# Kernel optimization log

Hardware: AMD Instinct MI355X
Metric: run time of the kernel (lower is better)

Reference implementation:

```python
import jax, jax.numpy as jnp
import numpy as np

EPS = 1e-6
N, D = 8192, 256


def setup_inputs() -> dict:
    key = jax.random.key(0)
    kq, kc = jax.random.split(key)
    # scale 0.05 keeps points inside the Poincare ball: c*||q||^2 ~ 0.06 << 1
    query = jax.random.normal(kq, (N, D), dtype=jnp.float32) * 0.05
    c = jnp.asarray(0.1, dtype=jnp.float32)  # learnable curvature param (init 0.1)
    return {"query": query, "c": c}


def reference(query, c):
    # Self-attention path of HyperbolicAttention (keys = values = query).
    clamp_c = jnp.maximum(c, EPS)
    # ||u-v||^2 = ||u||^2 + ||v||^2 - 2 u.v  (same math as explicit expand+subtract,
    # but via a single GEMM instead of an (N, N, D) intermediate)
    qn = jnp.sum(query * query, axis=-1)                       # (N,)
    gram = query @ query.T                                     # (N, N)
    diff_sq = jnp.maximum(qn[:, None] + qn[None, :] - 2.0 * gram, 0.0)
    t = jnp.maximum(1.0 - clamp_c * qn, EPS)                   # clamped 1 - c||x||^2
    denom = t[:, None] * t[None, :]                            # (N, N)
    arg = jnp.maximum(1.0 + 2.0 * clamp_c * diff_sq / denom, 1.0 + EPS) + EPS
    dist = jnp.arccosh(arg) / jnp.sqrt(clamp_c)                # (N, N)
    attn = jax.nn.softmax(-dist, axis=-1)                      # (N, N)
    return attn @ query                                        # (N, D)
```

## Files before the change

### kernel.cpp

```cpp
#include <hip/hip_runtime.h>
#include <math.h>

#define NN 8192
#define DD 256
#define EPSV 1e-6f
#define BM 128
#define BN 64
#define CSPLIT 4
#define COLS_PER_BLOCK (NN / CSPLIT)
#define NJT (COLS_PER_BLOCK / BN)
#define PSTR 72
#define TSTR 266
#define SMEM_BYTES (32768 * 3 + BM * PSTR * 2)

typedef __bf16 bf16x8 __attribute__((ext_vector_type(8)));
typedef float f32x16 __attribute__((ext_vector_type(16)));
typedef unsigned short ushort;
typedef unsigned int uint;


__device__ inline ushort f2bf(float x) {
    uint u = __float_as_uint(x);
    u += 0x7fffu + ((u >> 16) & 1u);
    return (ushort)(u >> 16);
}

__device__ inline void gload_lds16(const void* g, void* l) {
    __builtin_amdgcn_global_load_lds((const __attribute__((address_space(1))) uint*)g,
                                     (__attribute__((address_space(3))) uint*)l, 16, 0, 0);
}

__global__ void zero_kernel(float* __restrict__ p) {
    int i = blockIdx.x * 256 + threadIdx.x;
    ((float4*)p)[i] = make_float4(0.f, 0.f, 0.f, 0.f);
}

__global__ void prep_kernel(const float* __restrict__ q, const float* __restrict__ cp,
                            ushort* __restrict__ qbf, ushort* __restrict__ qbfT,
                            float* __restrict__ qn, float* __restrict__ itv2) {
    __shared__ ushort T[64 * TSTR];
    const int t = threadIdx.x;
    const int p0 = blockIdx.x * 64;
    const int pr = t >> 2, fq = t & 3;
    const int row = p0 + pr;
    const float4* src = (const float4*)(q + (size_t)row * DD + fq * 64);
    ushort loc[64];
    float ss = 0.f;
    #pragma unroll
    for (int i = 0; i < 16; ++i) {
        float4 v = src[i];
        ushort b0 = f2bf(v.x), b1 = f2bf(v.y), b2 = f2bf(v.z), b3 = f2bf(v.w);
        loc[i * 4 + 0] = b0; loc[i * 4 + 1] = b1; loc[i * 4 + 2] = b2; loc[i * 4 + 3] = b3;
        float r0 = __uint_as_float((uint)b0 << 16), r1 = __uint_as_float((uint)b1 << 16);
        float r2 = __uint_as_float((uint)b2 << 16), r3 = __uint_as_float((uint)b3 << 16);
        ss += r0 * r0 + r1 * r1 + r2 * r2 + r3 * r3;
    }
    #pragma unroll
    for (int k = 0; k < 8; ++k)
        *(uint4*)(qbf + (size_t)row * DD + (((fq * 8 + k) ^ (row & 7)) * 8)) = *(uint4*)&loc[k * 8];
    #pragma unroll
    for (int k = 0; k < 32; ++k)
        *(ushort2*)&T[pr * TSTR + fq * 64 + k * 2] = *(ushort2*)&loc[k * 2];
    ss += __shfl_xor(ss, 1, 64);
    ss += __shfl_xor(ss, 2, 64);
    if (fq == 0) {
        float cc = fmaxf(cp[0], EPSV);
        qn[row] = ss;
        float tt = fmaxf(1.0f - cc * ss, EPSV);
        itv2[row] = sqrtf(2.0f * cc) / tt;
    }
    __syncthreads();
    #pragma unroll
    for (int pass = 0; pass < 4; ++pass) {
        int f = pass * 64 + (t >> 2);
        int quarter = t & 3;
        ushort tmp[16];
        #pragma unroll
        for (int i = 0; i < 16; ++i) tmp[i] = T[(quarter * 16 + i) * TSTR + f];
        *(uint4*)(qbfT + (size_t)f * NN + p0 + quarter * 16) = *(uint4*)&tmp[0];
        *(uint4*)(qbfT + (size_t)f * NN + p0 + quarter * 16 + 8) = *(uint4*)&tmp[8];
    }
}

__global__ __launch_bounds__(512, 2) void flash_kernel(
    const ushort* __restrict__ qbf, const ushort* __restrict__ qbfT,
    const float* __restrict__ cp, const float* __restrict__ qn,
    const float* __restrict__ itv2, float* __restrict__ Oacc, float* __restrict__ lacc) {
    extern __shared__ char smem[];
    ushort* Ktlds = (ushort*)(smem + 65536);
    ushort* Plds = (ushort*)(smem + 98304);

    const int tid = threadIdx.x;
    const int lane = tid & 63;
    const int w = tid >> 6;
    const int l31 = lane & 31;
    const int lhi = lane >> 5;
    const int qr = w >> 1;
    const int qc = w & 1;
    const int R0 = blockIdx.y * BM;
    const int C0 = blockIdx.x * COLS_PER_BLOCK;

    const float cc = fmaxf(cp[0], EPSV);
    const float rsc = rsqrtf(cc);

    const int rowA = R0 + qr * 32 + l31;
    const ushort* qrow = qbf + (size_t)rowA * DD;
    bf16x8 qa[16];
    #pragma unroll
    for (int kk = 0; kk < 16; ++kk) {
        int c = kk * 2 + lhi;
        qa[kk] = *(const bf16x8*)(qrow + ((c ^ (rowA & 7)) * 8));
    }

    float qnr16[16], itr16[16];
    #pragma unroll
    for (int r = 0; r < 16; ++r) {
        int row = R0 + qr * 32 + (r & 3) + 8 * (r >> 2) + 4 * lhi;
        qnr16[r] = qn[row];
        itr16[r] = itv2[row];
    }

    f32x16 o[4];
    #pragma unroll
    for (int ct = 0; ct < 4; ++ct)
        #pragma unroll
        for (int i = 0; i < 16; ++i) o[ct][i] = 0.f;
    float racc[16];
    #pragma unroll
    for (int r = 0; r < 16; ++r) racc[r] = 0.f;

    {
        const char* g = (const char*)(qbf + (size_t)C0 * DD);
        #pragma unroll
        for (int i = 0; i < 4; ++i) {
            int base = i * 8192 + w * 1024;
            gload_lds16(g + base + lane * 16, smem + base);
        }
    }

    #pragma unroll 1
    for (int jt = 0; jt < NJT; ++jt) {
        const int C = C0 + jt * BN;
        const ushort* Kc = (const ushort*)(smem + (jt & 1) * 32768);
        __syncthreads();

        if (jt + 1 < NJT) {
            const char* g = (const char*)(qbf + (size_t)(C + BN) * DD);
            char* dst = smem + ((jt + 1) & 1) * 32768;
            #pragma unroll
            for (int i = 0; i < 4; ++i) {
                int base = i * 8192 + w * 1024;
                gload_lds16(g + base + lane * 16, dst + base);
            }
        }
        {
            #pragma unroll
            for (int i = 0; i < 4; ++i) {
                int f0 = i * 64 + w * 8;
                int f = f0 + (lane >> 3);
                const char* g = (const char*)(qbfT + (size_t)f * NN + C) +
                                (((lane & 7) ^ (f & 7)) * 16);
                gload_lds16(g, (char*)Ktlds + f0 * 128);
            }
        }

        f32x16 s;
        #pragma unroll
        for (int i = 0; i < 16; ++i) s[i] = 0.f;
        const int jrow = qc * 32 + l31;
        const ushort* krow = Kc + jrow * DD;
        #pragma unroll
        for (int kk = 0; kk < 16; ++kk) {
            int c = kk * 2 + lhi;
            bf16x8 b = *(const bf16x8*)(krow + ((c ^ (jrow & 7)) * 8));
            s = __builtin_amdgcn_mfma_f32_32x32x16_bf16(qa[kk], b, s, 0, 0, 0);
        }

        {
            int J = C + jrow;
            float qnj = qn[J];
            float itj = itv2[J];
            #pragma unroll
            for (int r = 0; r < 16; ++r) {
                int mloc = qr * 32 + (r & 3) + 8 * (r >> 2) + 4 * lhi;
                float diff = fmaxf(qnr16[r] + qnj - 2.0f * s[r], 0.0f);
                float u = diff * itr16[r] * itj;
                float z = fmaxf(1.0f + u, 1.0f + EPSV) + EPSV;
                float y = z + sqrtf(fmaf(z, z, -1.0f));
                float p = __builtin_amdgcn_exp2f(-rsc * __builtin_amdgcn_logf(y));
                racc[r] += p;
                Plds[mloc * PSTR + jrow] = f2bf(p);
            }
        }
        __syncthreads();

        #pragma unroll
        for (int kt = 0; kt < 4; ++kt) {
            bf16x8 pa = *(const bf16x8*)&Plds[(qr * 32 + l31) * PSTR + kt * 16 + 8 * lhi];
            #pragma unroll
            for (int ct = 0; ct < 4; ++ct) {
                int f = qc * 128 + ct * 32 + l31;
                int cj = kt * 2 + lhi;
                bf16x8 vb = *(const bf16x8*)(Ktlds + f * 64 + (((cj ^ (f & 7))) * 8));
                o[ct] = __builtin_amdgcn_mfma_f32_32x32x16_bf16(pa, vb, o[ct], 0, 0, 0);
            }
        }
    }

    #pragma unroll
    for (int ct = 0; ct < 4; ++ct) {
        #pragma unroll
        for (int r = 0; r < 16; ++r) {
            int row = R0 + qr * 32 + (r & 3) + 8 * (r >> 2) + 4 * lhi;
            int d = qc * 128 + ct * 32 + l31;
            atomicAdd(&Oacc[(size_t)row * DD + d], o[ct][r]);
        }
    }
    #pragma unroll
    for (int off = 1; off <= 16; off <<= 1)
        #pragma unroll
        for (int r = 0; r < 16; ++r) racc[r] += __shfl_xor(racc[r], off, 64);
    if (l31 == 0) {
        #pragma unroll
        for (int r = 0; r < 16; ++r) {
            int row = R0 + qr * 32 + (r & 3) + 8 * (r >> 2) + 4 * lhi;
            atomicAdd(&lacc[row], racc[r]);
        }
    }
}

__global__ void norm_kernel(const float* __restrict__ Oacc, const float* __restrict__ lacc,
                            float* __restrict__ out) {
    int i = blockIdx.x * 256 + threadIdx.x;
    float4 v = ((const float4*)Oacc)[i];
    float inv = 1.0f / lacc[i >> 6];
    ((float4*)out)[i] = make_float4(v.x * inv, v.y * inv, v.z * inv, v.w * inv);
}

extern "C" void kernel_launch(void* const* d_in, const int* in_sizes, int n_in,
                              void* d_out, int out_size, void* d_ws, size_t ws_size,
                              hipStream_t stream) {
    (void)in_sizes; (void)n_in; (void)out_size; (void)ws_size;
    const float* q = (const float*)d_in[0];
    const float* cp = (const float*)d_in[1];
    float* out = (float*)d_out;
    float* ws = (float*)d_ws;
    float* Oacc = ws;
    float* lacc = ws + (size_t)NN * DD;
    float* qn = lacc + NN;
    float* itv2 = qn + NN;
    ushort* qbf = (ushort*)(itv2 + NN);
    ushort* qbfT = qbf + (size_t)NN * DD;

    (void)hipFuncSetAttribute((const void*)flash_kernel,
                              hipFuncAttributeMaxDynamicSharedMemorySize, SMEM_BYTES);

    zero_kernel<<<(NN * DD + NN) / 4 / 256, 256, 0, stream>>>(ws);
    prep_kernel<<<NN / 64, 256, 0, stream>>>(q, cp, qbf, qbfT, qn, itv2);
    flash_kernel<<<dim3(CSPLIT, NN / BM), 512, SMEM_BYTES, stream>>>(qbf, qbfT, cp, qn, itv2, Oacc, lacc);
    norm_kernel<<<(NN * DD / 4) / 256, 256, 0, stream>>>(Oacc, lacc, out);
}
```

Measured before the change: 205.6 us.

## Double-buffer transposed V tiles, retile PV GEMM, fuse zeroing into prep

The transposed-value tile is now double-buffered and prefetched one iteration ahead along with the key tile, so its global-to-LDS load no longer sits on the critical path before the PV MFMAs. The PV product is retiled so each wave computes a 2x2 block of 32x32 outputs, which reuses P and V fragments across MFMAs. The P buffer uses an XOR-swizzled layout instead of padding. The separate zero kernel is folded into the prep kernel to save a launch. The grid becomes 1D and the distance math is restructured with FMAs. LDS use rises to 144KB, which likely drops occupancy from 2 blocks to 1 per CU.

```diff
diff --git a/kernel.cpp b/kernel.cpp
--- a/kernel.cpp
+++ b/kernel.cpp
@@ -9,9 +9,8 @@
 #define CSPLIT 4
 #define COLS_PER_BLOCK (NN / CSPLIT)
 #define NJT (COLS_PER_BLOCK / BN)
-#define PSTR 72
 #define TSTR 266
-#define SMEM_BYTES (32768 * 3 + BM * PSTR * 2)
+#define SMEM_BYTES (65536 + 65536 + 16384)
 
 typedef __bf16 bf16x8 __attribute__((ext_vector_type(8)));
 typedef float f32x16 __attribute__((ext_vector_type(16)));
@@ -30,17 +29,19 @@
                                      (__attribute__((address_space(3))) uint*)l, 16, 0, 0);
 }
 
-__global__ void zero_kernel(float* __restrict__ p) {
-    int i = blockIdx.x * 256 + threadIdx.x;
-    ((float4*)p)[i] = make_float4(0.f, 0.f, 0.f, 0.f);
-}
-
 __global__ void prep_kernel(const float* __restrict__ q, const float* __restrict__ cp,
                             ushort* __restrict__ qbf, ushort* __restrict__ qbfT,
-                            float* __restrict__ qn, float* __restrict__ itv2) {
+                            float* __restrict__ qn, float* __restrict__ itv2,
+                            float* __restrict__ Oacc, float* __restrict__ lacc) {
     __shared__ ushort T[64 * TSTR];
     const int t = threadIdx.x;
-    const int p0 = blockIdx.x * 64;
+    const int b = blockIdx.x;
+    float4 z4 = make_float4(0.f, 0.f, 0.f, 0.f);
+    #pragma unroll
+    for (int i = 0; i < 16; ++i) ((float4*)Oacc)[b * 4096 + i * 256 + t] = z4;
+    if (t < 16) ((float4*)lacc)[b * 16 + t] = z4;
+
+    const int p0 = b * 64;
     const int pr = t >> 2, fq = t & 3;
     const int row = p0 + pr;
     const float4* src = (const float4*)(q + (size_t)row * DD + fq * 64);
@@ -87,8 +88,7 @@
     const float* __restrict__ cp, const float* __restrict__ qn,
     const float* __restrict__ itv2, float* __restrict__ Oacc, float* __restrict__ lacc) {
     extern __shared__ char smem[];
-    ushort* Ktlds = (ushort*)(smem + 65536);
-    ushort* Plds = (ushort*)(smem + 98304);
+    ushort* Plds = (ushort*)(smem + 131072);
 
     const int tid = threadIdx.x;
     const int lane = tid & 63;
@@ -97,11 +97,17 @@
     const int lhi = lane >> 5;
     const int qr = w >> 1;
     const int qc = w & 1;
-    const int R0 = blockIdx.y * BM;
-    const int C0 = blockIdx.x * COLS_PER_BLOCK;
+    const int qr2 = w >> 2;
+    const int fc = w & 3;
+
+    const int lid = blockIdx.x;
+    const int cs = lid & 3;
+    const int rb = lid >> 2;
+    const int R0 = rb * BM;
+    const int C0 = cs * COLS_PER_BLOCK;
 
     const float cc = fmaxf(cp[0], EPSV);
-    const float rsc = rsqrtf(cc);
+    const float nrsc = -rsqrtf(cc);
 
     const int rowA = R0 + qr * 32 + l31;
     const ushort* qrow = qbf + (size_t)rowA * DD;
@@ -120,11 +126,13 @@
         itr16[r] = itv2[row];
     }
 
-    f32x16 o[4];
-    #pragma unroll
-    for (int ct = 0; ct < 4; ++ct)
-        #pragma unroll
-        for (int i = 0; i < 16; ++i) o[ct][i] = 0.f;
+    f32x16 o[2][2];
+    #pragma unroll
+    for (int a = 0; a < 2; ++a)
+        #pragma unroll
+        for (int bb = 0; bb < 2; ++bb)
+            #pragma unroll
+            for (int i = 0; i < 16; ++i) o[a][bb][i] = 0.f;
     float racc[16];
     #pragma unroll
     for (int r = 0; r < 16; ++r) racc[r] = 0.f;
@@ -136,38 +144,49 @@
             int base = i * 8192 + w * 1024;
             gload_lds16(g + base + lane * 16, smem + base);
         }
+        #pragma unroll
+        for (int i = 0; i < 4; ++i) {
+            int f0 = i * 64 + w * 8;
+            int f = f0 + (lane >> 3);
+            const char* gk = (const char*)(qbfT + (size_t)f * NN + C0) +
+                             (((lane & 7) ^ (f & 7)) * 16);
+            gload_lds16(gk, smem + 65536 + f0 * 128);
+        }
     }
 
     #pragma unroll 1
     for (int jt = 0; jt < NJT; ++jt) {
         const int C = C0 + jt * BN;
-        const ushort* Kc = (const ushort*)(smem + (jt & 1) * 32768);
+        const int cur = jt & 1;
+        const ushort* Kc = (const ushort*)(smem + cur * 32768);
+        const ushort* Ktc = (const ushort*)(smem + 65536 + cur * 32768);
         __syncthreads();
 
         if (jt + 1 < NJT) {
+            const int nxt = cur ^ 1;
             const char* g = (const char*)(qbf + (size_t)(C + BN) * DD);
-            char* dst = smem + ((jt + 1) & 1) * 32768;
             #pragma unroll
             for (int i = 0; i < 4; ++i) {
                 int base = i * 8192 + w * 1024;
-                gload_lds16(g + base + lane * 16, dst + base);
-            }
-        }
-        {
+                gload_lds16(g + base + lane * 16, smem + nxt * 32768 + base);
+            }
             #pragma unroll
             for (int i = 0; i < 4; ++i) {
                 int f0 = i * 64 + w * 8;
                 int f = f0 + (lane >> 3);
-                const char* g = (const char*)(qbfT + (size_t)f * NN + C) +
-                                (((lane & 7) ^ (f & 7)) * 16);
-                gload_lds16(g, (char*)Ktlds + f0 * 128);
-            }
-        }
+                const char* gk = (const char*)(qbfT + (size_t)f * NN + C + BN) +
+                                 (((lane & 7) ^ (f & 7)) * 16);
+                gload_lds16(gk, smem + 65536 + nxt * 32768 + f0 * 128);
+            }
+        }
+
+        const int jrow = qc * 32 + l31;
+        const float qnj = qn[C + jrow];
+        const float itj = itv2[C + jrow];
 
         f32x16 s;
         #pragma unroll
         for (int i = 0; i < 16; ++i) s[i] = 0.f;
-        const int jrow = qc * 32 + l31;
         const ushort* krow = Kc + jrow * DD;
         #pragma unroll
         for (int kk = 0; kk < 16; ++kk) {
@@ -177,45 +196,58 @@
         }
 
         {
-            int J = C + jrow;
-            float qnj = qn[J];
-            float itj = itv2[J];
+            const int jchunk = jrow >> 3;
+            const int jlow = jrow & 7;
             #pragma unroll
             for (int r = 0; r < 16; ++r) {
+                float qsum = qnr16[r] + qnj;
+                float itrj = itr16[r] * itj;
+                float diff = fmaf(-2.0f, s[r], qsum);
+                float z = fmaf(diff, itrj, 1.0f);
+                z = fmaxf(z, 1.0f + EPSV) + EPSV;
+                float y = z + sqrtf(fmaf(z, z, -1.0f));
+                float p = __builtin_amdgcn_exp2f(nrsc * __builtin_amdgcn_logf(y));
+                racc[r] += p;
                 int mloc = qr * 32 + (r & 3) + 8 * (r >> 2) + 4 * lhi;
-                float diff = fmaxf(qnr16[r] + qnj - 2.0f * s[r], 0.0f);
-                float u = diff * itr16[r] * itj;
-                float z = fmaxf(1.0f + u, 1.0f + EPSV) + EPSV;
-                float y = z + sqrtf(fmaf(z, z, -1.0f));
-                float p = __builtin_amdgcn_exp2f(-rsc * __builtin_amdgcn_logf(y));
-                racc[r] += p;
-                Plds[mloc * PSTR + jrow] = f2bf(p);
+                int idx = mloc * 64 + ((jchunk ^ (mloc & 7)) * 8) + jlow;
+                ((__bf16*)Plds)[idx] = (__bf16)p;
             }
         }
         __syncthreads();
 
         #pragma unroll
         for (int kt = 0; kt < 4; ++kt) {
-            bf16x8 pa = *(const bf16x8*)&Plds[(qr * 32 + l31) * PSTR + kt * 16 + 8 * lhi];
-            #pragma unroll
-            for (int ct = 0; ct < 4; ++ct) {
-                int f = qc * 128 + ct * 32 + l31;
+            bf16x8 pa[2], vb[2];
+            #pragma unroll
+            for (int cq = 0; cq < 2; ++cq) {
+                int m = qr2 * 64 + cq * 32 + l31;
+                int chunk = (kt * 2 + lhi) ^ (m & 7);
+                pa[cq] = *(const bf16x8*)(Plds + m * 64 + chunk * 8);
+            }
+            #pragma unroll
+            for (int cf = 0; cf < 2; ++cf) {
+                int f = fc * 64 + cf * 32 + l31;
                 int cj = kt * 2 + lhi;
-                bf16x8 vb = *(const bf16x8*)(Ktlds + f * 64 + (((cj ^ (f & 7))) * 8));
-                o[ct] = __builtin_amdgcn_mfma_f32_32x32x16_bf16(pa, vb, o[ct], 0, 0, 0);
-            }
-        }
-    }
-
-    #pragma unroll
-    for (int ct = 0; ct < 4; ++ct) {
-        #pragma unroll
-        for (int r = 0; r < 16; ++r) {
-            int row = R0 + qr * 32 + (r & 3) + 8 * (r >> 2) + 4 * lhi;
-            int d = qc * 128 + ct * 32 + l31;
-            atomicAdd(&Oacc[(size_t)row * DD + d], o[ct][r]);
-        }
-    }
+                vb[cf] = *(const bf16x8*)(Ktc + f * 64 + ((cj ^ (f & 7)) * 8));
+            }
+            #pragma unroll
+            for (int cq = 0; cq < 2; ++cq)
+                #pragma unroll
+                for (int cf = 0; cf < 2; ++cf)
+                    o[cq][cf] = __builtin_amdgcn_mfma_f32_32x32x16_bf16(pa[cq], vb[cf], o[cq][cf], 0, 0, 0);
+        }
+    }
+
+    #pragma unroll
+    for (int cq = 0; cq < 2; ++cq)
+        #pragma unroll
+        for (int cf = 0; cf < 2; ++cf)
+            #pragma unroll
+            for (int r = 0; r < 16; ++r) {
+                int row = R0 + qr2 * 64 + cq * 32 + (r & 3) + 8 * (r >> 2) + 4 * lhi;
+                int d = fc * 64 + cf * 32 + l31;
+                atomicAdd(&Oacc[(size_t)row * DD + d], o[cq][cf][r]);
+            }
     #pragma unroll
     for (int off = 1; off <= 16; off <<= 1)
         #pragma unroll
@@ -255,8 +287,7 @@
     (void)hipFuncSetAttribute((const void*)flash_kernel,
                               hipFuncAttributeMaxDynamicSharedMemorySize, SMEM_BYTES);
 
-    zero_kernel<<<(NN * DD + NN) / 4 / 256, 256, 0, stream>>>(ws);
-    prep_kernel<<<NN / 64, 256, 0, stream>>>(q, cp, qbf, qbfT, qn, itv2);
-    flash_kernel<<<dim3(CSPLIT, NN / BM), 512, SMEM_BYTES, stream>>>(qbf, qbfT, cp, qn, itv2, Oacc, lacc);
+    prep_kernel<<<NN / 64, 256, 0, stream>>>(q, cp, qbf, qbfT, qn, itv2, Oacc, lacc);
+    flash_kernel<<<CSPLIT * (NN / BM), 512, SMEM_BYTES, stream>>>(qbf, qbfT, cp, qn, itv2, Oacc, lacc);
     norm_kernel<<<(NN * DD / 4) / 256, 256, 0, stream>>>(Oacc, lacc, out);
 }
```

Measured after the change: 219.9 us. 1.07x slower.
